# Performance work log

Hardware: AMD Instinct MI355X
Metric: run time of the kernel (lower is better)

## Reference

```python
import jax, jax.numpy as jnp
import numpy as np

B, L, DM = 16, 1024, 128
DK = DV = 32
HF, HG, HC, HP, HT, HA = 2, 2, 2, 2, 1, 2  # full, log, local, prob, FFT, auto heads
MA = 25          # series_decomp moving average window
WIN = 32         # local attention causal window
EPS = 1e-5
SCALE = float(1.0 / np.sqrt(DK))

_i = np.arange(L)[:, None]
_j = np.arange(L)[None, :]
_d = _i - _j
# log-sparse: attend to self and keys at power-of-two causal distances
LOG_MASK = jnp.asarray((_d == 0) | ((_d > 0) & ((_d & (_d - 1)) == 0)))
LOC_MASK = jnp.asarray((_d >= 0) & (_d < WIN))
# ProbSparse (Informer, factor=5): fixed sample indices, u = U_part
_U = min(int(5 * np.ceil(np.log(L))), L)
PROB_IDX = jnp.asarray(np.random.RandomState(0).randint(0, L, size=(L, _U)))
AUTO_K = int(np.log(L))  # AutoCorrelation factor=1


def _cconv(x, w, b, pad):
    # x [B,L,DM] -> conv over time in NCH layout; pad-left = causal (Conv pad=2 + Chomp1d(2))
    y = jax.lax.conv_general_dilated(x.swapaxes(1, 2), w, (1,), [(pad, 0)],
                                     dimension_numbers=('NCH', 'OIH', 'NCH'))
    return y + b[None, :, None]


def _heads(y, H, d):
    # faithful to torch: .view(B, L, H, d) applied to [B, C, L] conv output (memory reinterpret)
    return y.reshape(y.shape[0], L, H, d)


def _qkv(xq, xk, xv, wq, bq, wk, bk, wv, bv, H):
    Q = _heads(_cconv(xq, wq, bq, 2), H, DK)
    K = _heads(_cconv(xk, wk, bk, 2), H, DK)
    V = _heads(_cconv(xv, wv, bv, 0), H, DV)
    return Q, K, V


def _attn(Q, K, V, mask=None):
    s = jnp.einsum('blhe,bshe->bhls', Q, K) * SCALE
    if mask is not None:
        s = jnp.where(mask, s, -1e9)
    return jnp.einsum('bhls,bshd->blhd', jax.nn.softmax(s, axis=-1), V)


def _prob_attn(Q, K, V):
    q, k, v = Q.swapaxes(1, 2), K.swapaxes(1, 2), V.swapaxes(1, 2)  # [B,H,L,D]
    Ks = k[:, :, PROB_IDX]                                  # [B,H,L,U,D] sampled keys
    qk = jnp.einsum('bhld,bhlud->bhlu', q, Ks)
    M = qk.max(-1) - qk.sum(-1) / L                         # sparsity measure
    top = jax.lax.top_k(M, _U)[1]                           # [B,H,u] active queries
    qr = jnp.take_along_axis(q, top[..., None], axis=2)
    sc = jnp.einsum('bhud,bhsd->bhus', qr, k) * SCALE
    cu = jnp.einsum('bhus,bhsd->bhud', jax.nn.softmax(sc, -1), v)
    ctx = jnp.broadcast_to(v.mean(axis=2, keepdims=True), v.shape)  # lazy queries get mean(V)
    bi = jnp.arange(v.shape[0])[:, None, None]
    hi = jnp.arange(v.shape[1])[None, :, None]
    return ctx.at[bi, hi, top].set(cu).swapaxes(1, 2)


def _auto_corr(Q, K, V):
    q = Q.transpose(0, 2, 3, 1)  # [B,H,E,L]
    k = K.transpose(0, 2, 3, 1)
    v = V.transpose(0, 2, 3, 1)
    corr = jnp.fft.irfft(jnp.fft.rfft(q, axis=-1) * jnp.conj(jnp.fft.rfft(k, axis=-1)), n=L, axis=-1)
    mv = corr.mean(axis=1).mean(axis=1)                     # [B,L] mean over heads+channels
    idx = jax.lax.top_k(mv.mean(axis=0), AUTO_K)[1]         # shared top-k delays
    w = jax.nn.softmax(mv[:, idx], axis=-1)                 # [B,k]
    tt = jnp.arange(L)
    agg = jnp.zeros_like(v)
    for i in range(AUTO_K):
        agg = agg + v[..., (tt + idx[i]) % L] * w[:, i][:, None, None, None]
    return agg.transpose(0, 3, 1, 2)                        # [B,L,H,E]


def _mavg(x, k):
    # replicate-padded moving average (Autoformer series_decomp) via cumsum
    p = (k - 1) // 2
    xp = jnp.concatenate([jnp.repeat(x[:, :1], p, axis=1), x, jnp.repeat(x[:, -1:], p, axis=1)], axis=1)
    cs = jnp.cumsum(xp, axis=1)
    cs = jnp.concatenate([jnp.zeros_like(cs[:, :1]), cs], axis=1)
    return (cs[:, k:] - cs[:, :-k]) / k


def _forward(fl):
    (iq, ik, iv,
     wqf, bqf, wkf, bkf, wvf, bvf,
     wqg, bqg, wkg, bkg, wvg, bvg,
     wql, bql, wkl, bkl, wvl, bvl,
     wqp, bqp, wkp, bkp, wvp, bvp,
     wqa, bqa, wka, bka, wva, bva,
     wfft, bfft, wap, bap, was, bas, wfc) = fl
    ctx = []
    Q, K, V = _qkv(iq, ik, iv, wqf, bqf, wkf, bkf, wvf, bvf, HF)
    ctx.append(_attn(Q, K, V))
    Q, K, V = _qkv(iq, ik, iv, wqg, bqg, wkg, bkg, wvg, bvg, HG)
    ctx.append(_attn(Q, K, V, LOG_MASK))
    Q, K, V = _qkv(iq, ik, iv, wql, bql, wkl, bkl, wvl, bvl, HC)
    ctx.append(_attn(Q, K, V, LOC_MASK))
    Q, K, V = _qkv(iq, ik, iv, wqp, bqp, wkp, bkp, wvp, bvp, HP)
    ctx.append(_prob_attn(Q, K, V))
    cf = jnp.fft.fft(iq, axis=1).real                       # FFT branch
    ctx.append((cf @ wfft + bfft).reshape(B, L, HT, DV))
    Q, K, V = _qkv(iq, ik, iv, wqa, bqa, wka, bka, wva, bva, HA)
    ca = _auto_corr(Q, K, V).reshape(B, L, HA * DV) @ wap + bap
    ca = iq + ca                                            # residual (dropout=eval identity)
    ca = ca - _mavg(ca, MA)                                 # seasonal part of series_decomp
    ctx.append((ca @ was + bas).reshape(B, L, HA, DV))
    c = jnp.concatenate(ctx, axis=2).reshape(B, L, -1)
    out = c @ wfc + iq
    mu = out.mean(-1, keepdims=True)
    var = out.var(-1, keepdims=True)                        # fresh LayerNorm: weight=1, bias=0
    return (out - mu) / jnp.sqrt(var + EPS)


def setup_inputs() -> dict:
    ks = iter(jax.random.split(jax.random.key(0), 64))
    def n(shape, s=0.02):
        return jax.random.normal(next(ks), shape, dtype=jnp.float32) * s
    d = {}
    d['input_Q'] = jax.random.normal(next(ks), (B, L, DM), dtype=jnp.float32)
    d['input_K'] = jax.random.normal(next(ks), (B, L, DM), dtype=jnp.float32)
    d['input_V'] = jax.random.normal(next(ks), (B, L, DM), dtype=jnp.float32)
    for nm, H in [('full', HF), ('log', HG), ('loc', HC), ('prob', HP), ('auto', HA)]:
        d['wq_' + nm] = n((DK * H, DM, 3)); d['bq_' + nm] = n((DK * H,))
        d['wk_' + nm] = n((DK * H, DM, 3)); d['bk_' + nm] = n((DK * H,))
        d['wv_' + nm] = n((DV * H, DM, 1)); d['bv_' + nm] = n((DV * H,))
    d['w_fft'] = n((DM, DV * HT)); d['b_fft'] = n((DV * HT,))
    d['w_aproj'] = n((DV * HA, DM)); d['b_aproj'] = n((DM,))
    d['w_asize'] = n((DM, DV * HA)); d['b_asize'] = n((DV * HA,))
    d['w_fc'] = n(((HF + HG + HC + HP + HT + HA) * DV, DM))
    return d


def reference(input_Q, input_K, input_V, wq_full, bq_full, wk_full, bk_full, wv_full, bv_full, wq_log, bq_log, wk_log, bk_log, wv_log, bv_log, wq_loc, bq_loc, wk_loc, bk_loc, wv_loc, bv_loc, wq_prob, bq_prob, wk_prob, bk_prob, wv_prob, bv_prob, wq_auto, bq_auto, wk_auto, bk_auto, wv_auto, bv_auto, w_fft, b_fft, w_aproj, b_aproj, w_asize, b_asize, w_fc):
    return _forward((input_Q, input_K, input_V, wq_full, bq_full, wk_full, bk_full, wv_full, bv_full, wq_log, bq_log, wk_log, bk_log, wv_log, bv_log, wq_loc, bq_loc, wk_loc, bk_loc, wv_loc, bv_loc, wq_prob, bq_prob, wk_prob, bk_prob, wv_prob, bv_prob, wq_auto, bq_auto, wk_auto, bk_auto, wv_auto, bv_auto, w_fft, b_fft, w_aproj, b_aproj, w_asize, b_asize, w_fc))
```

## Files before the change

kernel.cpp:

```cpp
#include <hip/hip_runtime.h>
#include <hip/hip_bf16.h>
#include <math.h>

#define B_   16
#define L_   1024
#define SCALE_ 0.17677669529663687f

__global__ void mt_kernel(int* __restrict__ pidx) {
  __shared__ unsigned int mt[624];
  int tid = threadIdx.x;
  if (tid == 0) {
    unsigned int s = 0u;
    for (int i = 0; i < 624; ++i) {
      mt[i] = s;
      s = 1812433253u * (s ^ (s >> 30)) + (unsigned)(i + 1);
    }
  }
  __syncthreads();
  const unsigned int HI = 0x80000000u, LO = 0x7fffffffu, MM = 0x9908b0dfu;
  for (int blk = 0; blk < 58; ++blk) {
    unsigned int n0 = 0, n1 = 0, n2 = 0, old623 = 0;
    bool a0 = tid < 227, a2 = tid < 169;
    if (a0) {
      unsigned int y0 = (mt[tid] & HI) | (mt[tid + 1] & LO);
      n0 = mt[tid + 397] ^ (y0 >> 1) ^ ((y0 & 1u) ? MM : 0u);
      unsigned int y1 = (mt[tid + 227] & HI) | (mt[tid + 228] & LO);
      n1 = n0 ^ (y1 >> 1) ^ ((y1 & 1u) ? MM : 0u);
      if (a2) {
        unsigned int y2 = (mt[tid + 454] & HI) | (mt[tid + 455] & LO);
        n2 = n1 ^ (y2 >> 1) ^ ((y2 & 1u) ? MM : 0u);
      }
      if (tid == 169) old623 = mt[623];
    }
    __syncthreads();
    if (a0) {
      mt[tid] = n0;
      mt[tid + 227] = n1;
      if (a2) mt[tid + 454] = n2;
    }
    __syncthreads();
    if (tid == 169) {
      unsigned int y = (old623 & HI) | (mt[0] & LO);
      mt[623] = n1 ^ (y >> 1) ^ ((y & 1u) ? MM : 0u);
    }
    __syncthreads();
    for (int i = tid; i < 624; i += 256) {
      int g = blk * 624 + i;
      if (g < 35840) {
        unsigned int y = mt[i];
        y ^= y >> 11;
        y ^= (y << 7) & 0x9d2c5680u;
        y ^= (y << 15) & 0xefc60000u;
        y ^= y >> 18;
        pidx[g] = (int)(y & 1023u);
      }
    }
  }
}

__device__ __forceinline__ void conv_body(const float* __restrict__ x,
                                          const float* __restrict__ w,
                                          const float* __restrict__ bias,
                                          float* __restrict__ out,
                                          float* smem, int b, int t0, int tid, int is1) {
  int cp = tid & 31;
  int tg = tid >> 5;
  int tt0 = tg * 8;
  float acc0[8], acc1[8];
  float b0v = bias[cp], b1v = bias[cp + 32];
  #pragma unroll
  for (int j = 0; j < 8; ++j) { acc0[j] = b0v; acc1[j] = b1v; }
  if (!is1) {
    float* xs = smem;
    float* ws = smem + 8448;
    for (int i = tid; i < 66 * 128; i += 256) {
      int r = i >> 7, d = i & 127;
      int t = t0 - 2 + r;
      xs[r * 128 + d] = (t >= 0) ? x[(size_t)b * 131072 + (size_t)t * 128 + d] : 0.0f;
    }
    for (int dc = 0; dc < 128; dc += 16) {
      __syncthreads();
      {
        int row = tid >> 2, sub = tid & 3;
        const float* wsrc = w + row * 384 + dc * 3 + sub * 12;
        float* wdst = ws + row * 52 + sub * 12;
        #pragma unroll
        for (int k = 0; k < 12; ++k) wdst[k] = wsrc[k];
      }
      __syncthreads();
      #pragma unroll
      for (int dl = 0; dl < 16; dl += 4) {
        int d0 = dc + dl;
        float4 xr[10];
        #pragma unroll
        for (int r = 0; r < 10; ++r) xr[r] = *(const float4*)&xs[(tt0 + r) * 128 + d0];
        float4 wa0 = *(const float4*)&ws[cp * 52 + dl * 3];
        float4 wa1 = *(const float4*)&ws[cp * 52 + dl * 3 + 4];
        float4 wa2 = *(const float4*)&ws[cp * 52 + dl * 3 + 8];
        float4 wb0 = *(const float4*)&ws[(cp + 32) * 52 + dl * 3];
        float4 wb1 = *(const float4*)&ws[(cp + 32) * 52 + dl * 3 + 4];
        float4 wb2 = *(const float4*)&ws[(cp + 32) * 52 + dl * 3 + 8];
        float w0r[12] = {wa0.x, wa0.y, wa0.z, wa0.w, wa1.x, wa1.y, wa1.z, wa1.w,
                         wa2.x, wa2.y, wa2.z, wa2.w};
        float w1r[12] = {wb0.x, wb0.y, wb0.z, wb0.w, wb1.x, wb1.y, wb1.z, wb1.w,
                         wb2.x, wb2.y, wb2.z, wb2.w};
        #pragma unroll
        for (int j = 0; j < 8; ++j) {
          float a0 = acc0[j], a1 = acc1[j];
          #pragma unroll
          for (int k = 0; k < 3; ++k) {
            float4 xv = xr[j + k];
            a0 = fmaf(w0r[0 + k], xv.x, a0);
            a0 = fmaf(w0r[3 + k], xv.y, a0);
            a0 = fmaf(w0r[6 + k], xv.z, a0);
            a0 = fmaf(w0r[9 + k], xv.w, a0);
            a1 = fmaf(w1r[0 + k], xv.x, a1);
            a1 = fmaf(w1r[3 + k], xv.y, a1);
            a1 = fmaf(w1r[6 + k], xv.z, a1);
            a1 = fmaf(w1r[9 + k], xv.w, a1);
          }
          acc0[j] = a0; acc1[j] = a1;
        }
      }
    }
  } else {
    float* xs = smem;
    float* ws = smem + 8192;
    for (int i = tid; i < 64 * 128; i += 256) {
      int r = i >> 7, d = i & 127;
      xs[r * 128 + d] = x[(size_t)b * 131072 + (size_t)(t0 + r) * 128 + d];
    }
    for (int dc = 0; dc < 128; dc += 32) {
      __syncthreads();
      {
        int row = tid >> 2, sub = tid & 3;
        const float* wsrc = w + row * 128 + dc + sub * 8;
        float* wdst = ws + row * 36 + sub * 8;
        #pragma unroll
        for (int k = 0; k < 8; ++k) wdst[k] = wsrc[k];
      }
      __syncthreads();
      #pragma unroll
      for (int dl = 0; dl < 32; dl += 4) {
        int d0 = dc + dl;
        float4 wv0 = *(const float4*)&ws[cp * 36 + dl];
        float4 wv1 = *(const float4*)&ws[(cp + 32) * 36 + dl];
        #pragma unroll
        for (int j = 0; j < 8; ++j) {
          float4 xv = *(const float4*)&xs[(tt0 + j) * 128 + d0];
          float a0 = acc0[j], a1 = acc1[j];
          a0 = fmaf(wv0.x, xv.x, a0);
          a0 = fmaf(wv0.y, xv.y, a0);
          a0 = fmaf(wv0.z, xv.z, a0);
          a0 = fmaf(wv0.w, xv.w, a0);
          a1 = fmaf(wv1.x, xv.x, a1);
          a1 = fmaf(wv1.y, xv.y, a1);
          a1 = fmaf(wv1.z, xv.z, a1);
          a1 = fmaf(wv1.w, xv.w, a1);
          acc0[j] = a0; acc1[j] = a1;
        }
      }
    }
  }
  float* op0 = out + (size_t)b * 65536 + (size_t)cp * 1024 + t0 + tt0;
  float* op1 = out + (size_t)b * 65536 + (size_t)(cp + 32) * 1024 + t0 + tt0;
  *(float4*)op0 = make_float4(acc0[0], acc0[1], acc0[2], acc0[3]);
  *(float4*)(op0 + 4) = make_float4(acc0[4], acc0[5], acc0[6], acc0[7]);
  *(float4*)op1 = make_float4(acc1[0], acc1[1], acc1[2], acc1[3]);
  *(float4*)(op1 + 4) = make_float4(acc1[4], acc1[5], acc1[6], acc1[7]);
}

__global__ __launch_bounds__(256, 3)
void qkv_conv_kernel(const float* __restrict__ xq, const float* __restrict__ xk,
                     const float* __restrict__ xv,
                     const float* __restrict__ wq, const float* __restrict__ bq,
                     const float* __restrict__ wk, const float* __restrict__ bk,
                     const float* __restrict__ wv, const float* __restrict__ bv,
                     float* __restrict__ qo, float* __restrict__ ko,
                     float* __restrict__ vo) {
  __shared__ float smem[11776];
  int which = blockIdx.z;
  const float* x = (which == 0) ? xq : (which == 1) ? xk : xv;
  const float* w = (which == 0) ? wq : (which == 1) ? wk : wv;
  const float* bias = (which == 0) ? bq : (which == 1) ? bk : bv;
  float* out = (which == 0) ? qo : (which == 1) ? ko : vo;
  conv_body(x, w, bias, out, smem, blockIdx.y, blockIdx.x * 64, threadIdx.x, which == 2);
}

struct ConvArgs {
  const float* x[3];
  const float* w[15];
  const float* bia[15];
  float* outbase;
};
__global__ __launch_bounds__(256, 3)
void qkv_conv_all(ConvArgs a) {
  __shared__ float smem[11776];
  int z = blockIdx.z;
  int which = z % 3;
  float* out = a.outbase + (size_t)z * 1048576;
  conv_body(a.x[which], a.w[z], a.bia[z], out, smem, blockIdx.y, blockIdx.x * 64,
            threadIdx.x, which == 2);
}

__global__ __launch_bounds__(128, 2)
void attn_full_part(const float* __restrict__ Q, const float* __restrict__ K,
                    const float* __restrict__ V, float* __restrict__ part,
                    int stile, int nstage) {
  __shared__ float Ks[128][32];
  __shared__ float Vs[128][32];
  int bh = blockIdx.z, b = bh >> 1, h = bh & 1;
  int tid = threadIdx.x;
  int l0 = blockIdx.x * 256 + tid;
  int s0 = blockIdx.y * stile;
  const float* Kb = K + (size_t)b * 65536 + h * 32;
  const float* Vb = V + (size_t)b * 65536 + h * 32;
  const float* Qb0 = Q + (size_t)b * 65536 + h * 32 + (size_t)l0 * 64;
  const float* Qb1 = Qb0 + 128 * 64;
  float qa[32], qb[32];
  #pragma unroll
  for (int i = 0; i < 8; ++i) {
    float4 v4 = ((const float4*)Qb0)[i];
    qa[4*i] = v4.x; qa[4*i+1] = v4.y; qa[4*i+2] = v4.z; qa[4*i+3] = v4.w;
    float4 w4 = ((const float4*)Qb1)[i];
    qb[4*i] = w4.x; qb[4*i+1] = w4.y; qb[4*i+2] = w4.z; qb[4*i+3] = w4.w;
  }
  float oa[32], ob[32];
  #pragma unroll
  for (int d = 0; d < 32; ++d) { oa[d] = 0.0f; ob[d] = 0.0f; }
  float ssa = 0.0f, ssb = 0.0f;
  for (int st = 0; st < nstage; ++st) {
    __syncthreads();
    int sb = s0 + st * 128;
    for (int i = tid; i < 1024; i += 128) {
      int r = i >> 3, d4 = i & 7;
      ((float4*)&Ks[r][0])[d4] = *(const float4*)(Kb + (size_t)(sb + r) * 64 + d4 * 4);
      ((float4*)&Vs[r][0])[d4] = *(const float4*)(Vb + (size_t)(sb + r) * 64 + d4 * 4);
    }
    __syncthreads();
    for (int s = 0; s < 128; s += 2) {
      const float4* kp0 = (const float4*)&Ks[s][0];
      const float4* kp1 = (const float4*)&Ks[s + 1][0];
      float a0 = 0, a1 = 0, a2 = 0, a3 = 0;
      float c0 = 0, c1 = 0, c2 = 0, c3 = 0;
      float e0 = 0, e1 = 0, e2 = 0, e3 = 0;
      float g0 = 0, g1 = 0, g2 = 0, g3 = 0;
      #pragma unroll
      for (int i = 0; i < 8; ++i) {
        float4 k0 = kp0[i], k1 = kp1[i];
        float qx = qa[4*i], qy = qa[4*i+1], qz = qa[4*i+2], qw = qa[4*i+3];
        a0 = fmaf(qx, k0.x, a0); a1 = fmaf(qy, k0.y, a1);
        a2 = fmaf(qz, k0.z, a2); a3 = fmaf(qw, k0.w, a3);
        c0 = fmaf(qx, k1.x, c0); c1 = fmaf(qy, k1.y, c1);
        c2 = fmaf(qz, k1.z, c2); c3 = fmaf(qw, k1.w, c3);
        qx = qb[4*i]; qy = qb[4*i+1]; qz = qb[4*i+2]; qw = qb[4*i+3];
        e0 = fmaf(qx, k0.x, e0); e1 = fmaf(qy, k0.y, e1);
        e2 = fmaf(qz, k0.z, e2); e3 = fmaf(qw, k0.w, e3);
        g0 = fmaf(qx, k1.x, g0); g1 = fmaf(qy, k1.y, g1);
        g2 = fmaf(qz, k1.z, g2); g3 = fmaf(qw, k1.w, g3);
      }
      float p0a = __expf(((a0 + a1) + (a2 + a3)) * SCALE_);
      float p1a = __expf(((c0 + c1) + (c2 + c3)) * SCALE_);
      float p0b = __expf(((e0 + e1) + (e2 + e3)) * SCALE_);
      float p1b = __expf(((g0 + g1) + (g2 + g3)) * SCALE_);
      ssa += p0a + p1a;
      ssb += p0b + p1b;
      const float4* vp0 = (const float4*)&Vs[s][0];
      const float4* vp1 = (const float4*)&Vs[s + 1][0];
      #pragma unroll
      for (int i = 0; i < 8; ++i) {
        float4 v0 = vp0[i], v1 = vp1[i];
        oa[4*i]   = fmaf(p0a, v0.x, fmaf(p1a, v1.x, oa[4*i]));
        oa[4*i+1] = fmaf(p0a, v0.y, fmaf(p1a, v1.y, oa[4*i+1]));
        oa[4*i+2] = fmaf(p0a, v0.z, fmaf(p1a, v1.z, oa[4*i+2]));
        oa[4*i+3] = fmaf(p0a, v0.w, fmaf(p1a, v1.w, oa[4*i+3]));
        ob[4*i]   = fmaf(p0b, v0.x, fmaf(p1b, v1.x, ob[4*i]));
        ob[4*i+1] = fmaf(p0b, v0.y, fmaf(p1b, v1.y, ob[4*i+1]));
        ob[4*i+2] = fmaf(p0b, v0.z, fmaf(p1b, v1.z, ob[4*i+2]));
        ob[4*i+3] = fmaf(p0b, v0.w, fmaf(p1b, v1.w, ob[4*i+3]));
      }
    }
  }
  float* pp = part + (((size_t)bh * gridDim.y + blockIdx.y) * 1024 + l0) * 36;
  #pragma unroll
  for (int i = 0; i < 8; ++i)
    ((float4*)pp)[i] = make_float4(oa[4*i], oa[4*i+1], oa[4*i+2], oa[4*i+3]);
  pp[32] = ssa;
  pp = part + (((size_t)bh * gridDim.y + blockIdx.y) * 1024 + l0 + 128) * 36;
  #pragma unroll
  for (int i = 0; i < 8; ++i)
    ((float4*)pp)[i] = make_float4(ob[4*i], ob[4*i+1], ob[4*i+2], ob[4*i+3]);
  pp[32] = ssb;
}

__global__ void attn_full_comb(const float* __restrict__ part, float* __restrict__ cbuf,
                               int nsplit) {
  int idx = blockIdx.x * 128 + threadIdx.x;
  int bh = idx >> 10, l = idx & 1023;
  int b = bh >> 1, h = bh & 1;
  float S = 0.0f;
  float o[32];
  #pragma unroll
  for (int d = 0; d < 32; ++d) o[d] = 0.0f;
  for (int j = 0; j < nsplit; ++j) {
    const float* pp = part + (((size_t)bh * nsplit + j) * 1024 + l) * 36;
    S += pp[32];
    #pragma unroll
    for (int i = 0; i < 8; ++i) {
      float4 v4 = ((const float4*)pp)[i];
      o[4*i] += v4.x; o[4*i+1] += v4.y; o[4*i+2] += v4.z; o[4*i+3] += v4.w;
    }
  }
  float inv = 1.0f / S;
  float* cc = cbuf + ((size_t)b * 1024 + l) * 352 + 0 + h * 32;
  #pragma unroll
  for (int d = 0; d < 32; ++d) cc[d] = o[d] * inv;
}

__global__ void attn_log_kernel(const float* __restrict__ Q, const float* __restrict__ K,
                                const float* __restrict__ V, float* __restrict__ cbuf) {
  int idx = blockIdx.x * 128 + threadIdx.x;
  int bh = idx >> 10, l = idx & 1023;
  int b = bh >> 1, h = bh & 1;
  const float* Qb = Q + (size_t)b * 65536 + h * 32;
  const float* Kb = K + (size_t)b * 65536 + h * 32;
  const float* Vb = V + (size_t)b * 65536 + h * 32;
  float q[32];
  #pragma unroll
  for (int i = 0; i < 8; ++i) {
    float4 v4 = ((const float4*)(Qb + (size_t)l * 64))[i];
    q[4*i] = v4.x; q[4*i+1] = v4.y; q[4*i+2] = v4.z; q[4*i+3] = v4.w;
  }
  float o[32];
  #pragma unroll
  for (int d = 0; d < 32; ++d) o[d] = 0.0f;
  float ssum = 0.0f;
  #pragma unroll
  for (int j = 0; j < 11; ++j) {
    int off = (j == 0) ? 0 : (1 << (j - 1));
    if (off <= l) {
      int s = l - off;
      const float4* kp = (const float4*)(Kb + (size_t)s * 64);
      float a0 = 0, a1 = 0, a2 = 0, a3 = 0;
      #pragma unroll
      for (int i = 0; i < 8; ++i) {
        float4 kv = kp[i];
        a0 = fmaf(q[4*i], kv.x, a0);
        a1 = fmaf(q[4*i+1], kv.y, a1);
        a2 = fmaf(q[4*i+2], kv.z, a2);
        a3 = fmaf(q[4*i+3], kv.w, a3);
      }
      float p = __expf(((a0 + a1) + (a2 + a3)) * SCALE_);
      ssum += p;
      const float4* vp = (const float4*)(Vb + (size_t)s * 64);
      #pragma unroll
      for (int i = 0; i < 8; ++i) {
        float4 vv = vp[i];
        o[4*i]   = fmaf(p, vv.x, o[4*i]);
        o[4*i+1] = fmaf(p, vv.y, o[4*i+1]);
        o[4*i+2] = fmaf(p, vv.z, o[4*i+2]);
        o[4*i+3] = fmaf(p, vv.w, o[4*i+3]);
      }
    }
  }
  float inv = 1.0f / ssum;
  float* cc = cbuf + ((size_t)b * 1024 + l) * 352 + 64 + h * 32;
  #pragma unroll
  for (int d = 0; d < 32; ++d) cc[d] = o[d] * inv;
}

__global__ void attn_loc_kernel(const float* __restrict__ Q, const float* __restrict__ K,
                                const float* __restrict__ V, float* __restrict__ cbuf) {
  int idx = blockIdx.x * 128 + threadIdx.x;
  int bh = idx >> 10, l = idx & 1023;
  int b = bh >> 1, h = bh & 1;
  const float* Qb = Q + (size_t)b * 65536 + h * 32;
  const float* Kb = K + (size_t)b * 65536 + h * 32;
  const float* Vb = V + (size_t)b * 65536 + h * 32;
  float q[32];
  #pragma unroll
  for (int i = 0; i < 8; ++i) {
    float4 v4 = ((const float4*)(Qb + (size_t)l * 64))[i];
    q[4*i] = v4.x; q[4*i+1] = v4.y; q[4*i+2] = v4.z; q[4*i+3] = v4.w;
  }
  float o[32];
  #pragma unroll
  for (int d = 0; d < 32; ++d) o[d] = 0.0f;
  float ssum = 0.0f;
  int jlo = (l >= 31) ? 0 : (31 - l);
  for (int j = jlo; j < 32; ++j) {
    int s = l - 31 + j;
    const float4* kp = (const float4*)(Kb + (size_t)s * 64);
    float a0 = 0, a1 = 0, a2 = 0, a3 = 0;
    #pragma unroll
    for (int i = 0; i < 8; ++i) {
      float4 kv = kp[i];
      a0 = fmaf(q[4*i], kv.x, a0);
      a1 = fmaf(q[4*i+1], kv.y, a1);
      a2 = fmaf(q[4*i+2], kv.z, a2);
      a3 = fmaf(q[4*i+3], kv.w, a3);
    }
    float p = __expf(((a0 + a1) + (a2 + a3)) * SCALE_);
    ssum += p;
    const float4* vp = (const float4*)(Vb + (size_t)s * 64);
    #pragma unroll
    for (int i = 0; i < 8; ++i) {
      float4 vv = vp[i];
      o[4*i]   = fmaf(p, vv.x, o[4*i]);
      o[4*i+1] = fmaf(p, vv.y, o[4*i+1]);
      o[4*i+2] = fmaf(p, vv.z, o[4*i+2]);
      o[4*i+3] = fmaf(p, vv.w, o[4*i+3]);
    }
  }
  float inv = 1.0f / ssum;
  float* cc = cbuf + ((size_t)b * 1024 + l) * 352 + 128 + h * 32;
  #pragma unroll
  for (int d = 0; d < 32; ++d) cc[d] = o[d] * inv;
}

__global__ void prob_m_kernel(const float* __restrict__ Q, const float* __restrict__ K,
                              const int* __restrict__ pidx, float* __restrict__ Mbuf) {
  int idx = blockIdx.x * 128 + threadIdx.x;
  int bh = idx >> 10, l = idx & 1023;
  int b = bh >> 1, h = bh & 1;
  const float* Qb = Q + (size_t)b * 65536 + h * 32;
  const float* Kb = K + (size_t)b * 65536 + h * 32;
  float q[32];
  #pragma unroll
  for (int i = 0; i < 8; ++i) {
    float4 v4 = ((const float4*)(Qb + (size_t)l * 64))[i];
    q[4*i] = v4.x; q[4*i+1] = v4.y; q[4*i+2] = v4.z; q[4*i+3] = v4.w;
  }
  float mx = -1e30f, sm = 0.0f;
  for (int u = 0; u < 35; ++u) {
    int ki = pidx[l * 35 + u];
    const float4* kp = (const float4*)(Kb + (size_t)ki * 64);
    float a0 = 0, a1 = 0, a2 = 0, a3 = 0;
    #pragma unroll
    for (int i = 0; i < 8; ++i) {
      float4 kv = kp[i];
      a0 = fmaf(q[4*i], kv.x, a0);
      a1 = fmaf(q[4*i+1], kv.y, a1);
      a2 = fmaf(q[4*i+2], kv.z, a2);
      a3 = fmaf(q[4*i+3], kv.w, a3);
    }
    float s = (a0 + a1) + (a2 + a3);
    mx = fmaxf(mx, s);
    sm += s;
  }
  Mbuf[(size_t)bh * 1024 + l] = mx - sm * (1.0f / 1024.0f);
}

__global__ void top35_kernel(const float* __restrict__ Mbuf, int* __restrict__ sel) {
  int bh = blockIdx.x;
  int lane = threadIdx.x;
  float v[16];
  const float* Mb = Mbuf + (size_t)bh * 1024 + lane * 16;
  #pragma unroll
  for (int k = 0; k < 16; ++k) v[k] = Mb[k];
  for (int it = 0; it < 35; ++it) {
    float bv = -1e30f; int bi = 0;
    #pragma unroll
    for (int k = 0; k < 16; ++k)
      if (v[k] > bv) { bv = v[k]; bi = k; }
    int gidx = lane * 16 + bi;
    #pragma unroll
    for (int off = 32; off > 0; off >>= 1) {
      float ov = __shfl_down(bv, off, 64);
      int og = __shfl_down(gidx, off, 64);
      if (ov > bv || (ov == bv && og < gidx)) { bv = ov; gidx = og; }
    }
    gidx = __shfl(gidx, 0, 64);
    if (lane == 0) sel[bh * 35 + it] = gidx;
    if ((gidx >> 4) == lane) {
      int kk = gidx & 15;
      #pragma unroll
      for (int k = 0; k < 16; ++k)
        if (k == kk) v[k] = -1e30f;
    }
  }
}

__global__ void prob_fill_kernel(const float* __restrict__ V, float* __restrict__ cbuf) {
  __shared__ float red[256];
  __shared__ float vm[32];
  int bh = blockIdx.x, b = bh >> 1, h = bh & 1;
  int tid = threadIdx.x;
  int d = tid & 31, ch = tid >> 5;
  const float* Vb = V + (size_t)b * 65536 + h * 32;
  float s = 0.0f;
  for (int ss = ch * 128; ss < ch * 128 + 128; ++ss) s += Vb[(size_t)ss * 64 + d];
  red[tid] = s;
  __syncthreads();
  if (ch == 0) {
    float t = 0.0f;
    for (int c = 0; c < 8; ++c) t += red[c * 32 + d];
    vm[d] = t * (1.0f / 1024.0f);
  }
  __syncthreads();
  for (int i = tid; i < 1024 * 32; i += 256) {
    int l = i >> 5, dd = i & 31;
    cbuf[((size_t)b * 1024 + l) * 352 + 192 + h * 32 + dd] = vm[dd];
  }
}

// ... 172 lines not shown
    float s = 0.0f;
    #pragma unroll
    for (int j = 0; j < 6; ++j) { vals[j] = __expf(vals[j] - mx); s += vals[j]; }
    #pragma unroll
    for (int j = 0; j < 6; ++j) w6[b * 6 + j] = vals[j] / s;
  }
}

__global__ void auto_agg_kernel(const float* __restrict__ Va, const float* __restrict__ iq,
                                const float* __restrict__ wap, const float* __restrict__ bap,
                                const int* __restrict__ idx6, const float* __restrict__ w6,
                                float* __restrict__ ca) {
  __shared__ float aggs[16][64];
  __shared__ float w6s[6];
  __shared__ int id6[6];
  int b = blockIdx.y, t0 = blockIdx.x * 16;
  int tid = threadIdx.x;
  if (tid < 6) { w6s[tid] = w6[b * 6 + tid]; id6[tid] = idx6[tid]; }
  __syncthreads();
  const float* Vb = Va + (size_t)b * 65536;
  for (int i = tid; i < 1024; i += 256) {
    int tl = i >> 6, c = i & 63;
    int t = t0 + tl;
    float s = 0.0f;
    #pragma unroll
    for (int j = 0; j < 6; ++j)
      s += w6s[j] * Vb[(size_t)((t + id6[j]) & 1023) * 64 + c];
    aggs[tl][c] = s;
  }
  __syncthreads();
  int dm = tid & 127, tp = tid >> 7;
  float acc[8];
  #pragma unroll
  for (int r = 0; r < 8; ++r) {
    int t = t0 + tp * 8 + r;
    acc[r] = bap[dm] + iq[((size_t)b * 1024 + t) * 128 + dm];
  }
  for (int c = 0; c < 64; ++c) {
    float wv = wap[c * 128 + dm];
    #pragma unroll
    for (int r = 0; r < 8; ++r) acc[r] += aggs[tp * 8 + r][c] * wv;
  }
  #pragma unroll
  for (int r = 0; r < 8; ++r)
    ca[((size_t)b * 1024 + t0 + tp * 8 + r) * 128 + dm] = acc[r];
}

__global__ void auto_ma_kernel(const float* __restrict__ ca, const float* __restrict__ was,
                               const float* __restrict__ bas, float* __restrict__ cbuf) {
  __shared__ float cas[40][128];
  __shared__ float diff[16][128];
  int b = blockIdx.y, t0 = blockIdx.x * 16;
  int tid = threadIdx.x;
  for (int i = tid; i < 40 * 128; i += 256) {
    int r = i >> 7, d = i & 127;
    int t = t0 - 12 + r;
    t = (t < 0) ? 0 : ((t > 1023) ? 1023 : t);
    cas[r][d] = ca[((size_t)b * 1024 + t) * 128 + d];
  }
  __syncthreads();
  int d = tid & 127, hf = tid >> 7;
  int tl0 = hf * 8;
  float s = 0.0f;
  #pragma unroll
  for (int w = 0; w < 25; ++w) s += cas[tl0 + w][d];
  #pragma unroll
  for (int k = 0; k < 8; ++k) {
    int tl = tl0 + k;
    diff[tl][d] = cas[tl + 12][d] - s * (1.0f / 25.0f);
    if (k < 7) s += cas[tl + 25][d] - cas[tl][d];
  }
  __syncthreads();
  int j = tid & 63, tq = tid >> 6;
  float acc[4];
  #pragma unroll
  for (int r = 0; r < 4; ++r) acc[r] = bas[j];
  for (int dd = 0; dd < 128; ++dd) {
    float wv = was[dd * 64 + j];
    #pragma unroll
    for (int r = 0; r < 4; ++r) acc[r] += diff[tq * 4 + r][dd] * wv;
  }
  #pragma unroll
  for (int r = 0; r < 4; ++r)
    cbuf[((size_t)b * 1024 + t0 + tq * 4 + r) * 352 + 288 + j] = acc[r];
}

__global__ void fftY_kernel(const float* __restrict__ x, const float* __restrict__ wfft,
                            float* __restrict__ Y) {
  __shared__ float xs[64][128];
  __shared__ float ws[32][129];
  int b = blockIdx.y, t0 = blockIdx.x * 64;
  int tid = threadIdx.x;
  for (int i = tid; i < 64 * 128; i += 256) {
    int r = i >> 7, d = i & 127;
    xs[r][d] = x[(size_t)b * 131072 + (size_t)(t0 + r) * 128 + d];
  }
  for (int i = tid; i < 4096; i += 256) {
    int d = i >> 5, j = i & 31;
    ws[j][d] = wfft[i];
  }
  __syncthreads();
  int j = tid & 31, tt0 = (tid >> 5) * 8;
  float acc[8];
  #pragma unroll
  for (int r = 0; r < 8; ++r) acc[r] = 0.0f;
  for (int d0 = 0; d0 < 128; d0 += 4) {
    float w0 = ws[j][d0], w1 = ws[j][d0 + 1], w2 = ws[j][d0 + 2], w3 = ws[j][d0 + 3];
    #pragma unroll
    for (int r = 0; r < 8; ++r) {
      float4 xv = *(const float4*)&xs[tt0 + r][d0];
      float a = acc[r];
      a = fmaf(w0, xv.x, a);
      a = fmaf(w1, xv.y, a);
      a = fmaf(w2, xv.z, a);
      a = fmaf(w3, xv.w, a);
      acc[r] = a;
    }
  }
  #pragma unroll
  for (int r = 0; r < 8; ++r)
    Y[((size_t)b * 1024 + t0 + tt0 + r) * 32 + j] = acc[r];
}

__global__ void fftT_kernel(const float* __restrict__ Y, const float* __restrict__ bfft,
                            float* __restrict__ cbuf) {
  __shared__ float ys[256 * 32];
  __shared__ float altred[8][32];
  int b = blockIdx.y, fbase = blockIdx.x * 64;
  int tid = threadIdx.x;
  int fi = tid & 31, jg = tid >> 5, j0 = jg * 4;
  int f0 = fbase + fi * 2;
  const float TWO_PI_N = 6.283185307179586476925f / 1024.0f;
  float ca0, sa0, ca1, sa1;
  sincosf(TWO_PI_N * (float)f0, &sa0, &ca0);
  sincosf(TWO_PI_N * (float)(f0 + 1), &sa1, &ca1);
  float cr0 = 1.0f, ci0 = 0.0f, cr1 = 1.0f, ci1 = 0.0f;
  float4 acc0 = make_float4(0.f, 0.f, 0.f, 0.f);
  float4 acc1 = make_float4(0.f, 0.f, 0.f, 0.f);
  bool do512 = (blockIdx.x == 0);
  int aj = tid & 31, arow = tid >> 5;
  float alt = 0.0f;
  for (int chk = 0; chk < 4; ++chk) {
    __syncthreads();
    const float4* Yp = (const float4*)(Y + ((size_t)b * 1024 + chk * 256) * 32);
    for (int i = tid; i < 2048; i += 256) ((float4*)ys)[i] = Yp[i];
    __syncthreads();
    for (int tl = 0; tl < 256; ++tl) {
      float4 yv = *(const float4*)&ys[tl * 32 + j0];
      acc0.x = fmaf(cr0, yv.x, acc0.x);
      acc0.y = fmaf(cr0, yv.y, acc0.y);
      acc0.z = fmaf(cr0, yv.z, acc0.z);
      acc0.w = fmaf(cr0, yv.w, acc0.w);
      acc1.x = fmaf(cr1, yv.x, acc1.x);
      acc1.y = fmaf(cr1, yv.y, acc1.y);
      acc1.z = fmaf(cr1, yv.z, acc1.z);
      acc1.w = fmaf(cr1, yv.w, acc1.w);
      float nr0 = cr0 * ca0 - ci0 * sa0;
      float ni0 = cr0 * sa0 + ci0 * ca0;
      cr0 = nr0; ci0 = ni0;
      float nr1 = cr1 * ca1 - ci1 * sa1;
      float ni1 = cr1 * sa1 + ci1 * ca1;
      cr1 = nr1; ci1 = ni1;
    }
    if (do512) {
      int tb = arow * 32;
      #pragma unroll 8
      for (int k = 0; k < 32; ++k) {
        float y = ys[(tb + k) * 32 + aj];
        alt += ((tb + k) & 1) ? -y : y;
      }
    }
  }
  float b0 = bfft[j0], b1 = bfft[j0 + 1], b2 = bfft[j0 + 2], b3 = bfft[j0 + 3];
  float* cc0 = cbuf + ((size_t)b * 1024 + f0) * 352 + 256 + j0;
  cc0[0] = acc0.x + b0; cc0[1] = acc0.y + b1; cc0[2] = acc0.z + b2; cc0[3] = acc0.w + b3;
  float* cc1 = cbuf + ((size_t)b * 1024 + f0 + 1) * 352 + 256 + j0;
  cc1[0] = acc1.x + b0; cc1[1] = acc1.y + b1; cc1[2] = acc1.z + b2; cc1[3] = acc1.w + b3;
  if (f0 > 0) {
    float* cm0 = cbuf + ((size_t)b * 1024 + (1024 - f0)) * 352 + 256 + j0;
    cm0[0] = acc0.x + b0; cm0[1] = acc0.y + b1; cm0[2] = acc0.z + b2; cm0[3] = acc0.w + b3;
  }
  {
    float* cm1 = cbuf + ((size_t)b * 1024 + (1024 - f0 - 1)) * 352 + 256 + j0;
    cm1[0] = acc1.x + b0; cm1[1] = acc1.y + b1; cm1[2] = acc1.z + b2; cm1[3] = acc1.w + b3;
  }
  if (do512) {
    altred[arow][aj] = alt;
    __syncthreads();
    if (tid < 32) {
      float s = 0.0f;
      #pragma unroll
      for (int r = 0; r < 8; ++r) s += altred[r][tid];
      cbuf[((size_t)b * 1024 + 512) * 352 + 256 + tid] = s + bfft[tid];
    }
  }
}

__global__ void fc_ln_kernel(const float* __restrict__ cbuf, const float* __restrict__ wfc,
                             const float* __restrict__ iq, float* __restrict__ out) {
  __shared__ float cs[16][352];
  __shared__ float os[16][128];
  int b = blockIdx.y, t0 = blockIdx.x * 16;
  int tid = threadIdx.x;
  for (int i = tid; i < 16 * 352; i += 256) {
    int r = i / 352, col = i % 352;
    cs[r][col] = cbuf[((size_t)b * 1024 + t0 + r) * 352 + col];
  }
  __syncthreads();
  int j = tid & 127, half = tid >> 7;
  float acc[8];
  #pragma unroll
  for (int k = 0; k < 8; ++k)
    acc[k] = iq[((size_t)b * 1024 + t0 + half * 8 + k) * 128 + j];
  for (int i = 0; i < 352; ++i) {
    float wv = wfc[i * 128 + j];
    #pragma unroll
    for (int k = 0; k < 8; ++k) acc[k] += cs[half * 8 + k][i] * wv;
  }
  #pragma unroll
  for (int k = 0; k < 8; ++k) os[half * 8 + k][j] = acc[k];
  __syncthreads();
  int wid = tid >> 6, lane = tid & 63;
  for (int rr = 0; rr < 4; ++rr) {
    int r = wid * 4 + rr;
    float x0 = os[r][lane], x1 = os[r][lane + 64];
    float s1 = x0 + x1;
    float s2 = x0 * x0 + x1 * x1;
    #pragma unroll
    for (int k = 32; k > 0; k >>= 1) {
      s1 += __shfl_xor(s1, k, 64);
      s2 += __shfl_xor(s2, k, 64);
    }
    float mean = s1 * (1.0f / 128.0f);
    float var = s2 * (1.0f / 128.0f) - mean * mean;
    float rstd = 1.0f / sqrtf(var + 1e-5f);
    float* op = out + ((size_t)b * 1024 + t0 + r) * 128;
    op[lane] = (x0 - mean) * rstd;
    op[lane + 64] = (x1 - mean) * rstd;
  }
}

extern "C" void kernel_launch(void* const* d_in, const int* in_sizes, int n_in,
                              void* d_out, int out_size, void* d_ws, size_t ws_size,
                              hipStream_t stream) {
  (void)in_sizes; (void)n_in; (void)out_size;
  const float* inQ = (const float*)d_in[0];
  const float* inK = (const float*)d_in[1];
  const float* inV = (const float*)d_in[2];
  const float *wq[5], *bq[5], *wk[5], *bk[5], *wv[5], *bv[5];
  for (int br = 0; br < 5; ++br) {
    wq[br] = (const float*)d_in[3 + br * 6 + 0];
    bq[br] = (const float*)d_in[3 + br * 6 + 1];
    wk[br] = (const float*)d_in[3 + br * 6 + 2];
    bk[br] = (const float*)d_in[3 + br * 6 + 3];
    wv[br] = (const float*)d_in[3 + br * 6 + 4];
    bv[br] = (const float*)d_in[3 + br * 6 + 5];
  }
  const float* wfft = (const float*)d_in[33];
  const float* bfft = (const float*)d_in[34];
  const float* wap  = (const float*)d_in[35];
  const float* bap  = (const float*)d_in[36];
  const float* was  = (const float*)d_in[37];
  const float* bas  = (const float*)d_in[38];
  const float* wfc  = (const float*)d_in[39];
  float* out = (float*)d_out;

  bool mega = ws_size >= (size_t)128 * 1024 * 1024;
  int nsplit = (ws_size >= (size_t)76 * 1024 * 1024) ? 8 : 4;
  int stile = 1024 / nsplit;
  int nstage = stile / 128;

  char* wsb = (char*)d_ws;
  size_t off = 0;
  auto alloc = [&](size_t bytes) -> void* {
    void* p = wsb + off;
    off += (bytes + 255) & ~(size_t)255;
    return p;
  };
  int*   pidx = (int*)  alloc((size_t)35840 * 4);
  float* qkvall = (float*)alloc((size_t)(mega ? 15 : 3) * 1048576 * 4);
  float* cbuf = (float*)alloc((size_t)16 * 1024 * 352 * 4);
  float* fpart = (float*)alloc((size_t)32 * nsplit * 1024 * 36 * 4);
  float* Mbuf = (float*)alloc((size_t)32 * 1024 * 4);
  int*   sel  = (int*)  alloc((size_t)32 * 35 * 4);
  float* mvb  = (float*)alloc((size_t)16 * 1024 * 4);
  int*   idx6 = (int*)  alloc(64);
  float* w6   = (float*)alloc((size_t)16 * 6 * 4);
  float* ppart = fpart;
  float* cab   = fpart;
  float* mpart = (float*)((char*)fpart + (size_t)8 * 1024 * 1024);
  float* Ybuf  = (float*)((char*)fpart + (size_t)12 * 1024 * 1024);

  mt_kernel<<<1, 256, 0, stream>>>(pidx);

  if (mega) {
    ConvArgs ca;
    ca.x[0] = inQ; ca.x[1] = inK; ca.x[2] = inV;
    for (int br = 0; br < 5; ++br) {
      ca.w[br * 3 + 0] = wq[br]; ca.bia[br * 3 + 0] = bq[br];
      ca.w[br * 3 + 1] = wk[br]; ca.bia[br * 3 + 1] = bk[br];
      ca.w[br * 3 + 2] = wv[br]; ca.bia[br * 3 + 2] = bv[br];
    }
    ca.outbase = qkvall;
    qkv_conv_all<<<dim3(16, 16, 15), 256, 0, stream>>>(ca);
  }
  auto bufs = [&](int br, float*& qb, float*& kb, float*& vb) {
    int bi = mega ? br : 0;
    qb = qkvall + (size_t)(bi * 3 + 0) * 1048576;
    kb = qkvall + (size_t)(bi * 3 + 1) * 1048576;
    vb = qkvall + (size_t)(bi * 3 + 2) * 1048576;
  };
  auto conv_branch = [&](int br, float* qb, float* kb, float* vb) {
    if (!mega)
      qkv_conv_kernel<<<dim3(16, 16, 3), 256, 0, stream>>>(
          inQ, inK, inV, wq[br], bq[br], wk[br], bk[br], wv[br], bv[br], qb, kb, vb);
  };
  float *qb, *kb, *vb;

  bufs(0, qb, kb, vb);
  conv_branch(0, qb, kb, vb);
  attn_full_part<<<dim3(4, nsplit, 32), 128, 0, stream>>>(qb, kb, vb, fpart, stile, nstage);
  attn_full_comb<<<256, 128, 0, stream>>>(fpart, cbuf, nsplit);

  bufs(1, qb, kb, vb);
  conv_branch(1, qb, kb, vb);
  attn_log_kernel<<<256, 128, 0, stream>>>(qb, kb, vb, cbuf);

  bufs(2, qb, kb, vb);
  conv_branch(2, qb, kb, vb);
  attn_loc_kernel<<<256, 128, 0, stream>>>(qb, kb, vb, cbuf);

  bufs(3, qb, kb, vb);
  conv_branch(3, qb, kb, vb);
  prob_m_kernel<<<256, 128, 0, stream>>>(qb, kb, pidx, Mbuf);
  top35_kernel<<<32, 64, 0, stream>>>(Mbuf, sel);
  prob_fill_kernel<<<32, 256, 0, stream>>>(vb, cbuf);
  prob_part_kernel<<<dim3(16, 32), 64, 0, stream>>>(qb, kb, vb, sel, ppart);
  prob_comb_kernel<<<18, 64, 0, stream>>>(ppart, sel, cbuf);

  bufs(4, qb, kb, vb);
  conv_branch(4, qb, kb, vb);
  auto_mv_part<<<dim3(64, 16), 128, 0, stream>>>(qb, kb, mpart);
  auto_mv_reduce<<<64, 256, 0, stream>>>(mpart, mvb);
  auto_top6_kernel<<<1, 64, 0, stream>>>(mvb, idx6, w6);
  auto_agg_kernel<<<dim3(64, 16), 256, 0, stream>>>(vb, inQ, wap, bap, idx6, w6, cab);
  auto_ma_kernel<<<dim3(64, 16), 256, 0, stream>>>(cab, was, bas, cbuf);

  fftY_kernel<<<dim3(16, 16), 256, 0, stream>>>(inQ, wfft, Ybuf);
  fftT_kernel<<<dim3(8, 16), 256, 0, stream>>>(Ybuf, bfft, cbuf);

  fc_ln_kernel<<<dim3(64, 16), 256, 0, stream>>>(cbuf, wfc, inQ, out);
}
```

Before: 688.9 us.

## Compute most QKV causal convolutions in fp16 with fdot2, keeping prob Q/K fp32

Replaces the all-fp32 QKV convolution launch with two kernels. One handles 13 of the 15 projections by converting inputs and weights to packed fp16 in shared memory and accumulating in fp32 with v_dot2 instructions. The other keeps the ProbSparse branch's Q and K projections in fp32, presumably because top-k query selection is sensitive to rounding. This is meant to cut ALU and LDS cost of the convolutions and raise occupancy, at the price of fp16 input rounding in most attention branches.

New measurement: 724.7 us. +5.2%, slower.

```diff
diff --git a/kernel.cpp b/kernel.cpp
--- a/kernel.cpp
+++ b/kernel.cpp
@@ -5,6 +5,12 @@
 #define B_   16
 #define L_   1024
 #define SCALE_ 0.17677669529663687f
+
+typedef _Float16 h2 __attribute__((ext_vector_type(2)));
+
+__device__ __forceinline__ float fdot2(unsigned int a, unsigned int b, float c) {
+  return __builtin_amdgcn_fdot2(__builtin_bit_cast(h2, a), __builtin_bit_cast(h2, b), c, false);
+}
 
 __global__ void mt_kernel(int* __restrict__ pidx) {
   __shared__ unsigned int mt[624];
@@ -193,14 +199,144 @@
   const float* bia[15];
   float* outbase;
 };
+
 __global__ __launch_bounds__(256, 3)
-void qkv_conv_all(ConvArgs a) {
+void qkv_conv_f32pair(ConvArgs a) {
   __shared__ float smem[11776];
-  int z = blockIdx.z;
+  int z = 9 + blockIdx.z;
+  float* out = a.outbase + (size_t)z * 1048576;
+  conv_body(a.x[z % 3], a.w[z], a.bia[z], out, smem, blockIdx.y, blockIdx.x * 64,
+            threadIdx.x, 0);
+}
+
+__global__ __launch_bounds__(256, 4)
+void qkv_conv_f16(ConvArgs a) {
+  __shared__ h2 smem2[7296];
+  const int zmap[13] = {0, 1, 2, 3, 4, 5, 6, 7, 8, 11, 12, 13, 14};
+  int z = zmap[blockIdx.z];
   int which = z % 3;
+  const float* x = a.x[which];
+  const float* w = a.w[z];
+  const float* bias = a.bia[z];
   float* out = a.outbase + (size_t)z * 1048576;
-  conv_body(a.x[which], a.w[z], a.bia[z], out, smem, blockIdx.y, blockIdx.x * 64,
-            threadIdx.x, which == 2);
+  int b = blockIdx.y, t0 = blockIdx.x * 64;
+  int tid = threadIdx.x;
+  int cp = tid & 31, tg = tid >> 5, tt0 = tg * 8;
+  float acc0[8], acc1[8];
+  float b0v = bias[cp], b1v = bias[cp + 32];
+  #pragma unroll
+  for (int j = 0; j < 8; ++j) { acc0[j] = b0v; acc1[j] = b1v; }
+
+  if (which < 2) {
+    h2* xs = smem2;
+    h2* ws = smem2 + 4224;
+    for (int i = tid; i < 66 * 64; i += 256) {
+      int r = i >> 6, p = i & 63;
+      int t = t0 - 2 + r;
+      float x0 = 0.0f, x1 = 0.0f;
+      if (t >= 0) {
+        const float* xp = x + (size_t)b * 131072 + (size_t)t * 128 + 2 * p;
+        x0 = xp[0]; x1 = xp[1];
+      }
+      h2 v; v[0] = (_Float16)x0; v[1] = (_Float16)x1;
+      xs[i] = v;
+    }
+    for (int dc = 0; dc < 128; dc += 32) {
+      __syncthreads();
+      {
+        int c = tid >> 2, quarter = tid & 3;
+        #pragma unroll
+        for (int fi = 0; fi < 12; ++fi) {
+          int f = quarter * 12 + fi;
+          int k = f >> 4, p = f & 15;
+          const float* wp = w + c * 384 + (dc + 2 * p) * 3 + k;
+          h2 v; v[0] = (_Float16)wp[0]; v[1] = (_Float16)wp[3];
+          ws[(c * 3 + k) * 16 + p] = v;
+        }
+      }
+      __syncthreads();
+      #pragma unroll
+      for (int dl = 0; dl < 4; ++dl) {
+        int p0 = (dc >> 1) + dl * 4;
+        uint4 xr[10];
+        #pragma unroll
+        for (int r = 0; r < 10; ++r)
+          xr[r] = *(const uint4*)&xs[(tt0 + r) * 64 + p0];
+        uint4 w0k[3], w1k[3];
+        #pragma unroll
+        for (int k = 0; k < 3; ++k) {
+          w0k[k] = *(const uint4*)&ws[(cp * 3 + k) * 16 + dl * 4];
+          w1k[k] = *(const uint4*)&ws[((cp + 32) * 3 + k) * 16 + dl * 4];
+        }
+        #pragma unroll
+        for (int j = 0; j < 8; ++j) {
+          float A0 = acc0[j], A1 = acc1[j];
+          #pragma unroll
+          for (int k = 0; k < 3; ++k) {
+            uint4 xv = xr[j + k];
+            A0 = fdot2(xv.x, w0k[k].x, A0);
+            A0 = fdot2(xv.y, w0k[k].y, A0);
+            A0 = fdot2(xv.z, w0k[k].z, A0);
+            A0 = fdot2(xv.w, w0k[k].w, A0);
+            A1 = fdot2(xv.x, w1k[k].x, A1);
+            A1 = fdot2(xv.y, w1k[k].y, A1);
+            A1 = fdot2(xv.z, w1k[k].z, A1);
+            A1 = fdot2(xv.w, w1k[k].w, A1);
+          }
+          acc0[j] = A0; acc1[j] = A1;
+        }
+      }
+    }
+  } else {
+    h2* xs = smem2;
+    h2* ws1 = smem2 + 4096;
+    for (int i = tid; i < 64 * 64; i += 256) {
+      int r = i >> 6, p = i & 63;
+      const float* xp = x + (size_t)b * 131072 + (size_t)(t0 + r) * 128 + 2 * p;
+      h2 v; v[0] = (_Float16)xp[0]; v[1] = (_Float16)xp[1];
+      xs[i] = v;
+    }
+    for (int dc = 0; dc < 128; dc += 32) {
+      __syncthreads();
+      {
+        int c = tid >> 2, quarter = tid & 3;
+        #pragma unroll
+        for (int pi = 0; pi < 4; ++pi) {
+          int p = quarter * 4 + pi;
+          const float* wp = w + c * 128 + dc + 2 * p;
+          h2 v; v[0] = (_Float16)wp[0]; v[1] = (_Float16)wp[1];
+          ws1[c * 16 + p] = v;
+        }
+      }
+      __syncthreads();
+      #pragma unroll
+      for (int dl = 0; dl < 4; ++dl) {
+        int p0 = (dc >> 1) + dl * 4;
+        uint4 wv0 = *(const uint4*)&ws1[cp * 16 + dl * 4];
+        uint4 wv1 = *(const uint4*)&ws1[(cp + 32) * 16 + dl * 4];
+        #pragma unroll
+        for (int j = 0; j < 8; ++j) {
+          uint4 xv = *(const uint4*)&xs[(tt0 + j) * 64 + p0];
+          float A0 = acc0[j], A1 = acc1[j];
+          A0 = fdot2(xv.x, wv0.x, A0);
+          A0 = fdot2(xv.y, wv0.y, A0);
+          A0 = fdot2(xv.z, wv0.z, A0);
+          A0 = fdot2(xv.w, wv0.w, A0);
+          A1 = fdot2(xv.x, wv1.x, A1);
+          A1 = fdot2(xv.y, wv1.y, A1);
+          A1 = fdot2(xv.z, wv1.z, A1);
+          A1 = fdot2(xv.w, wv1.w, A1);
+          acc0[j] = A0; acc1[j] = A1;
+        }
+      }
+    }
+  }
+  float* op0 = out + (size_t)b * 65536 + (size_t)cp * 1024 + t0 + tt0;
+  float* op1 = out + (size_t)b * 65536 + (size_t)(cp + 32) * 1024 + t0 + tt0;
+  *(float4*)op0 = make_float4(acc0[0], acc0[1], acc0[2], acc0[3]);
+  *(float4*)(op0 + 4) = make_float4(acc0[4], acc0[5], acc0[6], acc0[7]);
+  *(float4*)op1 = make_float4(acc1[0], acc1[1], acc1[2], acc1[3]);
+  *(float4*)(op1 + 4) = make_float4(acc1[4], acc1[5], acc1[6], acc1[7]);
 }
 
 __global__ __launch_bounds__(128, 2)
@@ -979,7 +1115,8 @@
       ca.w[br * 3 + 2] = wv[br]; ca.bia[br * 3 + 2] = bv[br];
     }
     ca.outbase = qkvall;
-    qkv_conv_all<<<dim3(16, 16, 15), 256, 0, stream>>>(ca);
+    qkv_conv_f16<<<dim3(16, 16, 13), 256, 0, stream>>>(ca);
+    qkv_conv_f32pair<<<dim3(16, 16, 2), 256, 0, stream>>>(ca);
   }
   auto bufs = [&](int br, float*& qb, float*& kb, float*& vb) {
     int bi = mega ? br : 0;
```

## Split mega QKV conv into specialized kernel-3 and kernel-1 launches

Applied to the files above, without the earlier changes.

Replaces the single generic conv launch over all 15 Q/K/V projections with two launches. A new register-tiled kernel handles the ten width-3 causal convs: each thread computes 4 channels by 8 timesteps, with input and weight chunks staged in shared memory and read as float4. The reused generic body handles the five width-1 V convs. This aims to raise arithmetic intensity in the dominant conv work, at the cost of an extra launch and higher register pressure.

New measurement: 666.2 us, median of 2. 1.03x faster.

```diff
diff --git a/kernel.cpp b/kernel.cpp
--- a/kernel.cpp
+++ b/kernel.cpp
@@ -193,14 +193,119 @@
   const float* bia[15];
   float* outbase;
 };
+
 __global__ __launch_bounds__(256, 3)
-void qkv_conv_all(ConvArgs a) {
+void conv1_mega(ConvArgs a) {
   __shared__ float smem[11776];
-  int z = blockIdx.z;
+  const int zmap[5] = {2, 5, 8, 11, 14};
+  int z = zmap[blockIdx.z];
+  float* out = a.outbase + (size_t)z * 1048576;
+  conv_body(a.x[2], a.w[z], a.bia[z], out, smem, blockIdx.y, blockIdx.x * 64,
+            threadIdx.x, 1);
+}
+
+__global__ __launch_bounds__(256, 3)
+void conv3_mega(ConvArgs a) {
+  __shared__ float xs[130 * 16];
+  __shared__ float ws[64 * 52];
+  const int zmap[10] = {0, 1, 3, 4, 6, 7, 9, 10, 12, 13};
+  int z = zmap[blockIdx.z];
   int which = z % 3;
+  const float* x = a.x[which];
+  const float* w = a.w[z];
+  const float* bias = a.bia[z];
   float* out = a.outbase + (size_t)z * 1048576;
-  conv_body(a.x[which], a.w[z], a.bia[z], out, smem, blockIdx.y, blockIdx.x * 64,
-            threadIdx.x, which == 2);
+  int b = blockIdx.y, t0 = blockIdx.x * 128;
+  int tid = threadIdx.x;
+  int cg = tid & 15;
+  int tg = tid >> 4;
+  int tt0 = tg * 8;
+  int c0 = cg, c1 = cg + 16, c2 = cg + 32, c3 = cg + 48;
+  float acc0[8], acc1[8], acc2[8], acc3[8];
+  {
+    float b0 = bias[c0], b1 = bias[c1], b2 = bias[c2], b3 = bias[c3];
+    #pragma unroll
+    for (int j = 0; j < 8; ++j) { acc0[j] = b0; acc1[j] = b1; acc2[j] = b2; acc3[j] = b3; }
+  }
+  for (int dc = 0; dc < 128; dc += 16) {
+    __syncthreads();
+    {
+      int row = tid >> 2, sub = tid & 3;
+      const float* wsrc = w + row * 384 + dc * 3 + sub * 12;
+      float* wdst = ws + row * 52 + sub * 12;
+      #pragma unroll
+      for (int k = 0; k < 12; ++k) wdst[k] = wsrc[k];
+    }
+    for (int i = tid; i < 520; i += 256) {
+      int row = i >> 2, db = i & 3;
+      int t = t0 - 2 + row;
+      float4 v = make_float4(0.f, 0.f, 0.f, 0.f);
+      if (t >= 0) v = *(const float4*)(x + (size_t)b * 131072 + (size_t)t * 128 + dc + db * 4);
+      *(float4*)&xs[row * 16 + db * 4] = v;
+    }
+    __syncthreads();
+    #pragma unroll
+    for (int dl = 0; dl < 16; dl += 4) {
+      float4 xr[10];
+      #pragma unroll
+      for (int r = 0; r < 10; ++r) xr[r] = *(const float4*)&xs[(tt0 + r) * 16 + dl];
+      float4 p0 = *(const float4*)&ws[c0 * 52 + dl * 3];
+      float4 p1 = *(const float4*)&ws[c0 * 52 + dl * 3 + 4];
+      float4 p2 = *(const float4*)&ws[c0 * 52 + dl * 3 + 8];
+      float w0r[12] = {p0.x, p0.y, p0.z, p0.w, p1.x, p1.y, p1.z, p1.w, p2.x, p2.y, p2.z, p2.w};
+      p0 = *(const float4*)&ws[c1 * 52 + dl * 3];
+      p1 = *(const float4*)&ws[c1 * 52 + dl * 3 + 4];
+      p2 = *(const float4*)&ws[c1 * 52 + dl * 3 + 8];
+      float w1r[12] = {p0.x, p0.y, p0.z, p0.w, p1.x, p1.y, p1.z, p1.w, p2.x, p2.y, p2.z, p2.w};
+      p0 = *(const float4*)&ws[c2 * 52 + dl * 3];
+      p1 = *(const float4*)&ws[c2 * 52 + dl * 3 + 4];
+      p2 = *(const float4*)&ws[c2 * 52 + dl * 3 + 8];
+      float w2r[12] = {p0.x, p0.y, p0.z, p0.w, p1.x, p1.y, p1.z, p1.w, p2.x, p2.y, p2.z, p2.w};
+      p0 = *(const float4*)&ws[c3 * 52 + dl * 3];
+      p1 = *(const float4*)&ws[c3 * 52 + dl * 3 + 4];
+      p2 = *(const float4*)&ws[c3 * 52 + dl * 3 + 8];
+      float w3r[12] = {p0.x, p0.y, p0.z, p0.w, p1.x, p1.y, p1.z, p1.w, p2.x, p2.y, p2.z, p2.w};
+      #pragma unroll
+      for (int j = 0; j < 8; ++j) {
+        float a0 = acc0[j], a1 = acc1[j], a2 = acc2[j], a3 = acc3[j];
+        #pragma unroll
+        for (int k = 0; k < 3; ++k) {
+          float4 xv = xr[j + k];
+          a0 = fmaf(w0r[0 + k], xv.x, a0);
+          a0 = fmaf(w0r[3 + k], xv.y, a0);
+          a0 = fmaf(w0r[6 + k], xv.z, a0);
+          a0 = fmaf(w0r[9 + k], xv.w, a0);
+          a1 = fmaf(w1r[0 + k], xv.x, a1);
+          a1 = fmaf(w1r[3 + k], xv.y, a1);
+          a1 = fmaf(w1r[6 + k], xv.z, a1);
+          a1 = fmaf(w1r[9 + k], xv.w, a1);
+          a2 = fmaf(w2r[0 + k], xv.x, a2);
+          a2 = fmaf(w2r[3 + k], xv.y, a2);
+          a2 = fmaf(w2r[6 + k], xv.z, a2);
+          a2 = fmaf(w2r[9 + k], xv.w, a2);
+          a3 = fmaf(w3r[0 + k], xv.x, a3);
+          a3 = fmaf(w3r[3 + k], xv.y, a3);
+          a3 = fmaf(w3r[6 + k], xv.z, a3);
+          a3 = fmaf(w3r[9 + k], xv.w, a3);
+        }
+        acc0[j] = a0; acc1[j] = a1; acc2[j] = a2; acc3[j] = a3;
+      }
+    }
+  }
+  size_t obase = (size_t)b * 65536 + t0 + tt0;
+  float* op;
+  op = out + obase + (size_t)c0 * 1024;
+  *(float4*)op = make_float4(acc0[0], acc0[1], acc0[2], acc0[3]);
+  *(float4*)(op + 4) = make_float4(acc0[4], acc0[5], acc0[6], acc0[7]);
+  op = out + obase + (size_t)c1 * 1024;
+  *(float4*)op = make_float4(acc1[0], acc1[1], acc1[2], acc1[3]);
+  *(float4*)(op + 4) = make_float4(acc1[4], acc1[5], acc1[6], acc1[7]);
+  op = out + obase + (size_t)c2 * 1024;
+  *(float4*)op = make_float4(acc2[0], acc2[1], acc2[2], acc2[3]);
+  *(float4*)(op + 4) = make_float4(acc2[4], acc2[5], acc2[6], acc2[7]);
+  op = out + obase + (size_t)c3 * 1024;
+  *(float4*)op = make_float4(acc3[0], acc3[1], acc3[2], acc3[3]);
+  *(float4*)(op + 4) = make_float4(acc3[4], acc3[5], acc3[6], acc3[7]);
 }
 
 __global__ __launch_bounds__(128, 2)
@@ -979,7 +1084,8 @@
       ca.w[br * 3 + 2] = wv[br]; ca.bia[br * 3 + 2] = bv[br];
     }
     ca.outbase = qkvall;
-    qkv_conv_all<<<dim3(16, 16, 15), 256, 0, stream>>>(ca);
+    conv3_mega<<<dim3(8, 16, 10), 256, 0, stream>>>(ca);
+    conv1_mega<<<dim3(16, 16, 5), 256, 0, stream>>>(ca);
   }
   auto bufs = [&](int br, float*& qb, float*& kb, float*& vb) {
     int bi = mega ? br : 0;
```
